# Optimization experiments

Hardware: AMD Instinct MI355X
Metric: run time of the kernel (lower is better)

The kernel has to match this reference:

```python
import jax, jax.numpy as jnp
import numpy as np

L, P = 8, 512
HID = 128
N_COARSE, N_FINE = 64, 128
LVIS_NEAR, LVIS_FAR = 1e-3, 0.5
S = 100.0  # 1 / fixed_s_recp


def _mlp_sdf(x, w0, b0, w1, b1, w2, b2, w3, b3):
    # x: [..., 3] -> sdf [...]
    h = jax.nn.relu(x @ w0 + b0)
    h = jax.nn.relu(h @ w1 + b1)
    h = jax.nn.relu(h @ w2 + b2)
    return (h @ w3 + b3)[..., 0]


def _sdf_to_w(sdf, s):
    # faithful to sdf_to_w: cdf -> alpha -> visibility weights via cumprod
    cdf = jax.nn.sigmoid(sdf * s)
    alpha = jnp.clip((cdf[..., :-1] - cdf[..., 1:]) / (cdf[..., :-1] + 1e-10), 0.0, None)
    ones = jnp.ones(alpha.shape[:-1] + (1,), alpha.dtype)
    shifted = jnp.concatenate([ones, 1.0 - alpha + 1e-10], axis=-1)
    return alpha * jnp.cumprod(shifted, axis=-1)[..., :-1]


def _sample_pdf(bins, weights, u):
    # standard NeRF importance sampling; bins [...,M+1], weights [...,M], u [...,N]
    weights = weights + 1e-5
    pdf = weights / jnp.sum(weights, axis=-1, keepdims=True)
    cdf = jnp.cumsum(pdf, axis=-1)
    cdf = jnp.concatenate([jnp.zeros_like(cdf[..., :1]), cdf], axis=-1)  # [...,M+1]
    # searchsorted (right) via broadcast compare: [...,N,M+1]
    inds = jnp.sum((u[..., None] >= cdf[..., None, :]).astype(jnp.int32), axis=-1)
    below = jnp.clip(inds - 1, 0, cdf.shape[-1] - 1)
    above = jnp.clip(inds, 0, cdf.shape[-1] - 1)
    cdf_b = jnp.take_along_axis(cdf, below, axis=-1)
    cdf_a = jnp.take_along_axis(cdf, above, axis=-1)
    bins_b = jnp.take_along_axis(bins, below, axis=-1)
    bins_a = jnp.take_along_axis(bins, above, axis=-1)
    denom = cdf_a - cdf_b
    denom = jnp.where(denom < 1e-5, jnp.ones_like(denom), denom)
    t = (u - cdf_b) / denom
    return bins_b + t * (bins_a - bins_b)


def setup_inputs() -> dict:
    key = jax.random.key(0)
    ks = jax.random.split(key, 8)

    def lin(k, fi, fo):
        return jax.random.normal(k, (fi, fo), jnp.float32) / jnp.sqrt(jnp.float32(fi))

    return {
        "pts": jax.random.normal(ks[0], (1, P, 3), jnp.float32) * 0.5,
        "light_posi": jax.random.normal(ks[1], (L, 3), jnp.float32) * 2.0,
        "u": jax.random.uniform(ks[2], (L, P, N_FINE), jnp.float32),
        "w0": lin(ks[3], 3, HID), "b0": jnp.zeros((HID,), jnp.float32),
        "w1": lin(ks[4], HID, HID), "b1": jnp.zeros((HID,), jnp.float32),
        "w2": lin(ks[5], HID, HID), "b2": jnp.zeros((HID,), jnp.float32),
        "w3": lin(ks[6], HID, 1), "b3": jnp.zeros((1,), jnp.float32),
    }


def reference(pts, light_posi, u, w0, b0, w1, b1, w2, b2, w3, b3):
    sdf = lambda x: _mlp_sdf(x, w0, b0, w1, b1, w2, b2, w3, b3)
    # pts: [1,P,3]; light_posi: [L,3]
    pts2l = light_posi[:, None, :] - pts  # [L,P,3]
    pts2l = pts2l / jnp.linalg.norm(pts2l, axis=-1, keepdims=True)
    t = jnp.linspace(0.0, 1.0 - 1.0 / N_COARSE, N_COARSE, dtype=jnp.float32)
    d_coarse = LVIS_NEAR * (1.0 - t) + LVIS_FAR * t  # [N_COARSE]
    d_coarse = jnp.broadcast_to(d_coarse, (pts2l.shape[0], pts.shape[1], N_COARSE))
    # coarse sample points: [L,P,Nc,3]
    pts_coarse = pts[:, :, None, :] + d_coarse[..., None] * pts2l[:, :, None, :]
    w_coarse = _sdf_to_w(sdf(pts_coarse), S)  # [L,P,Nc-1]
    d_fine = _sample_pdf(d_coarse, w_coarse, u)  # [L,P,Nf]
    d_all = jnp.sort(jnp.concatenate([d_coarse, d_fine], axis=-1), axis=-1)  # [L,P,Nc+Nf]
    pts_all = pts[:, :, None, :] + d_all[..., None] * pts2l[:, :, None, :]
    w_all = _sdf_to_w(sdf(pts_all), S)
    occu = jnp.sum(w_all, axis=-1)  # [L,P]
    return 1.0 - occu
```

## Files before the change

kernel.cpp:

```cpp
#include <hip/hip_runtime.h>
#include <math.h>

#define NL 8
#define NP 512
#define NC 64
#define NF 128
#define NALL 192
#define NRAY (NL * NP)
#define HID 128

typedef _Float16 half8 __attribute__((ext_vector_type(8)));
typedef _Float16 half4v __attribute__((ext_vector_type(4)));
typedef float floatx16 __attribute__((ext_vector_type(16)));

#define MFMA(a, b, c) __builtin_amdgcn_mfma_f32_32x32x16_f16((a), (b), (c), 0, 0, 0)

__device__ __forceinline__ float dcoarse_at(int i) {
    float t = (float)i * 0.015625f;
    return 1e-3f * (1.0f - t) + 0.5f * t;
}

__device__ __forceinline__ floatx16 fzero16() {
    floatx16 z;
#pragma unroll
    for (int i = 0; i < 16; ++i) z[i] = 0.f;
    return z;
}
__device__ __forceinline__ half8 hzero8() {
    half8 z;
#pragma unroll
    for (int i = 0; i < 8; ++i) z[i] = (_Float16)0.f;
    return z;
}

__global__ void prep_kernel(const float* __restrict__ w1, const float* __restrict__ w2,
                            _Float16* __restrict__ Wsp) {
    int f = blockIdx.x * 256 + threadIdx.x;
    int layer = blockIdx.y;
    const float* w = layer ? w2 : w1;
    int i = f & 7, l31 = (f >> 3) & 31, lhi = (f >> 8) & 1, ks = (f >> 9) & 7, jb = f >> 12;
    int j = jb * 32 + l31;
    int k = ks * 16 + lhi * 8 + i;
    float v = w[k * 128 + j];
    _Float16 hi = (_Float16)v;
    Wsp[(layer * 2 + 0) * 16384 + f] = hi;
    Wsp[(layer * 2 + 1) * 16384 + f] = (_Float16)(v - (float)hi);
}

template<int MODE, int FASTW>
__global__ __launch_bounds__(256, 2) void mlp_kernel(
    const float* __restrict__ pts, const float* __restrict__ lights,
    const float* __restrict__ d_all,
    const float* __restrict__ w0, const float* __restrict__ b0,
    const float* __restrict__ w1, const float* __restrict__ b1,
    const float* __restrict__ w2, const float* __restrict__ b2,
    const float* __restrict__ w3, const float* __restrict__ b3,
    const _Float16* __restrict__ Wsp,
    float* __restrict__ sdf_out)
{
    __shared__ __align__(16) _Float16 Hhi[128 * 128];
    __shared__ __align__(16) _Float16 Hlo[128 * 128];
    __shared__ _Float16 Xs[6 * 128];
    __shared__ float P2[2 * 128];

    const int tid = threadIdx.x;
    const int lane = tid & 63;
    const int wv = tid >> 6;
    const int jh = wv & 1, mh = wv >> 1;
    const int l31 = lane & 31, lhi = lane >> 5;
    const int base = blockIdx.x * 128;

    if (tid < 128) {
        int pt = base + tid;
        int ray; float d;
        if (MODE == 0) { ray = pt >> 6; d = dcoarse_at(pt & 63); }
        else           { ray = (int)((unsigned)pt / 192u); d = d_all[pt]; }
        int l = ray >> 9, p = ray & (NP - 1);
        float px = pts[p * 3 + 0], py = pts[p * 3 + 1], pz = pts[p * 3 + 2];
        float dx = lights[l * 3 + 0] - px, dy = lights[l * 3 + 1] - py, dz = lights[l * 3 + 2] - pz;
        float n = sqrtf(dx * dx + dy * dy + dz * dz);
        dx /= n; dy /= n; dz /= n;
        float xc[3] = { px + d * dx, py + d * dy, pz + d * dz };
#pragma unroll
        for (int c = 0; c < 3; ++c) {
            _Float16 h = (_Float16)xc[c];
            Xs[c * 128 + tid] = h;
            Xs[(3 + c) * 128 + tid] = (_Float16)(xc[c] - (float)h);
        }
    }
    __syncthreads();

    const int m0 = mh * 64;

    auto haddr = [&](int m, int k0) {
        return m * 128 + ((((k0 >> 3) ^ (m & 15)) << 3) | (k0 & 7));
    };

    auto store_tile = [&](const floatx16& a, int jt, int mt, const float* __restrict__ bias) {
        int m = m0 + mt * 32 + l31;
#pragma unroll
        for (int g = 0; g < 4; ++g) {
            int jg = jh * 64 + jt * 32 + 8 * g + 4 * lhi;
            half4v hq, lq;
#pragma unroll
            for (int q = 0; q < 4; ++q) {
                float v = fmaxf(a[g * 4 + q] + bias[jg + q], 0.f);
                _Float16 hi = (_Float16)v;
                hq[q] = hi;
                lq[q] = (_Float16)(v - (float)hi);
            }
            int ad = haddr(m, jg);
            *(half4v*)&Hhi[ad] = hq;
            *(half4v*)&Hlo[ad] = lq;
        }
    };

    floatx16 acc[2][2];

    {
        half8 a1h[2], a1l[2], bh1[2], bl1[2];
#pragma unroll
        for (int jt = 0; jt < 2; ++jt) { a1h[jt] = hzero8(); a1l[jt] = hzero8(); }
#pragma unroll
        for (int mt = 0; mt < 2; ++mt) { bh1[mt] = hzero8(); bl1[mt] = hzero8(); }
        if (lhi == 0) {
#pragma unroll
            for (int jt = 0; jt < 2; ++jt) {
                int j = jh * 64 + jt * 32 + l31;
#pragma unroll
                for (int c = 0; c < 3; ++c) {
                    float v = w0[c * 128 + j];
                    _Float16 hi = (_Float16)v;
                    a1h[jt][c] = hi;
                    a1l[jt][c] = (_Float16)(v - (float)hi);
                }
            }
#pragma unroll
            for (int mt = 0; mt < 2; ++mt) {
                int m = m0 + mt * 32 + l31;
#pragma unroll
                for (int c = 0; c < 3; ++c) {
                    bh1[mt][c] = Xs[c * 128 + m];
                    bl1[mt][c] = Xs[(3 + c) * 128 + m];
                }
            }
        }
#pragma unroll
        for (int jt = 0; jt < 2; ++jt)
#pragma unroll
            for (int mt = 0; mt < 2; ++mt) acc[jt][mt] = fzero16();
#pragma unroll
        for (int jt = 0; jt < 2; ++jt)
#pragma unroll
            for (int mt = 0; mt < 2; ++mt) acc[jt][mt] = MFMA(a1l[jt], bh1[mt], acc[jt][mt]);
#pragma unroll
        for (int jt = 0; jt < 2; ++jt)
#pragma unroll
            for (int mt = 0; mt < 2; ++mt) acc[jt][mt] = MFMA(a1h[jt], bl1[mt], acc[jt][mt]);
#pragma unroll
        for (int jt = 0; jt < 2; ++jt)
#pragma unroll
            for (int mt = 0; mt < 2; ++mt) acc[jt][mt] = MFMA(a1h[jt], bh1[mt], acc[jt][mt]);
#pragma unroll
        for (int jt = 0; jt < 2; ++jt)
#pragma unroll
            for (int mt = 0; mt < 2; ++mt) store_tile(acc[jt][mt], jt, mt, b0);
    }
    __syncthreads();

    auto ldA = [&](int L, int jt, int ks, half8& ah, half8& al) {
        if (FASTW) {
            int off = ((((jh * 2 + jt) * 8 + ks) * 2 + lhi) * 32 + l31) * 8;
            ah = *(const half8*)&Wsp[(L * 2 + 0) * 16384 + off];
            al = *(const half8*)&Wsp[(L * 2 + 1) * 16384 + off];
        } else {
            const float* w = L ? w2 : w1;
            int j = jh * 64 + jt * 32 + l31, k0 = ks * 16 + lhi * 8;
#pragma unroll
            for (int i = 0; i < 8; ++i) {
                float v = w[(k0 + i) * 128 + j];
                _Float16 hi = (_Float16)v;
                ah[i] = hi;
                al[i] = (_Float16)(v - (float)hi);
            }
        }
    };

    half8 bh[2][8], bl[2][8];

    auto gemm = [&](int L) {
#pragma unroll
        for (int mt = 0; mt < 2; ++mt) {
            int m = m0 + mt * 32 + l31;
#pragma unroll
            for (int ks = 0; ks < 8; ++ks) {
                int ad = haddr(m, ks * 16 + lhi * 8);
                bh[mt][ks] = *(const half8*)&Hhi[ad];
                bl[mt][ks] = *(const half8*)&Hlo[ad];
            }
        }
#pragma unroll
        for (int jt = 0; jt < 2; ++jt)
#pragma unroll
            for (int mt = 0; mt < 2; ++mt) acc[jt][mt] = fzero16();
#pragma unroll
        for (int ks = 0; ks < 8; ++ks) {
            half8 ah[2], al[2];
            ldA(L, 0, ks, ah[0], al[0]);
            ldA(L, 1, ks, ah[1], al[1]);
#pragma unroll
            for (int jt = 0; jt < 2; ++jt)
#pragma unroll
                for (int mt = 0; mt < 2; ++mt) acc[jt][mt] = MFMA(al[jt], bh[mt][ks], acc[jt][mt]);
#pragma unroll
            for (int jt = 0; jt < 2; ++jt)
#pragma unroll
                for (int mt = 0; mt < 2; ++mt) acc[jt][mt] = MFMA(ah[jt], bl[mt][ks], acc[jt][mt]);
#pragma unroll
            for (int jt = 0; jt < 2; ++jt)
#pragma unroll
                for (int mt = 0; mt < 2; ++mt) acc[jt][mt] = MFMA(ah[jt], bh[mt][ks], acc[jt][mt]);
        }
    };

    gemm(0);
    __syncthreads();
#pragma unroll
    for (int jt = 0; jt < 2; ++jt)
#pragma unroll
        for (int mt = 0; mt < 2; ++mt) store_tile(acc[jt][mt], jt, mt, b1);
    __syncthreads();

    gemm(1);
#pragma unroll
    for (int mt = 0; mt < 2; ++mt) {
        float p = 0.f;
#pragma unroll
        for (int jt = 0; jt < 2; ++jt)
#pragma unroll
            for (int g = 0; g < 4; ++g) {
                int jg = jh * 64 + jt * 32 + 8 * g + 4 * lhi;
#pragma unroll
                for (int q = 0; q < 4; ++q) {
                    float v = fmaxf(acc[jt][mt][g * 4 + q] + b2[jg + q], 0.f);
                    p = fmaf(v, w3[jg + q], p);
                }
            }
        p += __shfl_xor(p, 32);
        if (lane < 32) P2[jh * 128 + m0 + mt * 32 + l31] = p;
    }
    __syncthreads();
    if (tid < 128) sdf_out[base + tid] = b3[0] + P2[tid] + P2[128 + tid];
}

__global__ __launch_bounds__(256) void sample_kernel(
    const float* __restrict__ sdf_c, const float* __restrict__ u,
    float* __restrict__ d_all) {
    const int lane = threadIdx.x & 63, wv = threadIdx.x >> 6;
    const int ray = blockIdx.x * 4 + wv;

    float sv = sdf_c[ray * NC + lane];
    float c = 1.0f / (1.0f + expf(-100.0f * sv));
    float cn = __shfl_down(c, 1);
    bool valid = lane < 63;
    float a = valid ? fmaxf((c - cn) / (c + 1e-10f), 0.f) : 0.f;
    float sh = valid ? (1.f - a + 1e-10f) : 1.f;
    float ps = sh;
#pragma unroll
    for (int off = 1; off < 64; off <<= 1) { float o = __shfl_up(ps, off); if (lane >= off) ps *= o; }
    float T = __shfl_up(ps, 1);
    if (lane == 0) T = 1.f;
    float w = valid ? (a * T + 1e-5f) : 0.f;
    float wsum = w;
#pragma unroll
    for (int off = 1; off < 64; off <<= 1) wsum += __shfl_xor(wsum, off);
    float pdf = w / wsum;
    float cs = pdf;
#pragma unroll
    for (int off = 1; off < 64; off <<= 1) { float o = __shfl_up(cs, off); if (lane >= off) cs += o; }
    float cdfv = __shfl_up(cs, 1);
    if (lane == 0) cdfv = 0.f;

    float v[4];
    v[0] = dcoarse_at(lane);
    v[3] = __builtin_inff();
#pragma unroll
    for (int t = 0; t < 2; ++t) {
        float uu = u[ray * NF + t * 64 + lane];
        int lo = 0;
#pragma unroll
        for (int b = 32; b >= 1; b >>= 1) {
            float cm = __shfl(cdfv, lo + b);
            if (uu >= cm) lo += b;
        }
        int above = min(lo + 1, NC - 1);
        float cb = __shfl(cdfv, lo), ca = __shfl(cdfv, above);
        float bb = dcoarse_at(lo), ba = dcoarse_at(above);
        float denom = ca - cb;
        if (denom < 1e-5f) denom = 1.f;
        float tt = (uu - cb) / denom;
        v[1 + t] = bb + tt * (ba - bb);
    }

    for (int k = 2; k <= 256; k <<= 1) {
        for (int j = k >> 1; j > 0; j >>= 1) {
            if (j >= 64) {
                int tj = j >> 6;
#pragma unroll
                for (int t = 0; t < 4; ++t) {
                    if ((t & tj) == 0) {
                        int t2 = t ^ tj;
                        bool asc = (((t * 64) & k) == 0);
                        float x = v[t], y = v[t2];
                        bool sw = asc ? (x > y) : (x < y);
                        if (sw) { v[t] = y; v[t2] = x; }
                    }
                }
            } else {
#pragma unroll
                for (int t = 0; t < 4; ++t) {
                    int i = t * 64 + lane;
                    float other = __shfl_xor(v[t], j);
                    bool lower = (lane & j) == 0;
                    bool asc = ((i & k) == 0);
                    v[t] = (lower == asc) ? fminf(v[t], other) : fmaxf(v[t], other);
                }
            }
        }
    }
#pragma unroll
    for (int t = 0; t < 3; ++t) d_all[ray * NALL + t * 64 + lane] = v[t];
}

__global__ __launch_bounds__(256) void finish_kernel(
    const float* __restrict__ sdf_a, float* __restrict__ out) {
    int lane = threadIdx.x & 63, wv = threadIdx.x >> 6;
    int ray = blockIdx.x * 4 + wv;
    const float* S = sdf_a + (size_t)ray * NALL;
    float c[4];
#pragma unroll
    for (int t = 0; t < 4; ++t) {
        int i = lane * 3 + t;
        c[t] = (i < NALL) ? 1.0f / (1.0f + expf(-100.0f * S[i])) : 0.f;
    }
    float a[3], s[3];
#pragma unroll
    for (int t = 0; t < 3; ++t) {
        int i = lane * 3 + t;
        if (i < NALL - 1) {
            a[t] = fmaxf((c[t] - c[t + 1]) / (c[t] + 1e-10f), 0.f);
            s[t] = 1.f - a[t] + 1e-10f;
        } else { a[t] = 0.f; s[t] = 1.f; }
    }
    float chunk = s[0] * s[1] * s[2];
    float ps = chunk;
#pragma unroll
    for (int off = 1; off < 64; off <<= 1) {
        float o = __shfl_up(ps, off);
        if (lane >= off) ps *= o;
    }
    float T = __shfl_up(ps, 1);
    if (lane == 0) T = 1.f;
    float occ = a[0] * T;
    T *= s[0]; occ = fmaf(a[1], T, occ);
    T *= s[1]; occ = fmaf(a[2], T, occ);
#pragma unroll
    for (int off = 1; off < 64; off <<= 1) occ += __shfl_xor(occ, off);
    if (lane == 0) out[ray] = 1.f - occ;
}

extern "C" void kernel_launch(void* const* d_in, const int* in_sizes, int n_in,
                              void* d_out, int out_size, void* d_ws, size_t ws_size,
                              hipStream_t stream) {
    const float* pts = (const float*)d_in[0];
    const float* lights = (const float*)d_in[1];
    const float* u = (const float*)d_in[2];
    const float* w0 = (const float*)d_in[3];
    const float* b0 = (const float*)d_in[4];
    const float* w1 = (const float*)d_in[5];
    const float* b1 = (const float*)d_in[6];
    const float* w2 = (const float*)d_in[7];
    const float* b2 = (const float*)d_in[8];
    const float* w3 = (const float*)d_in[9];
    const float* b3 = (const float*)d_in[10];
    float* out = (float*)d_out;

    float* ws = (float*)d_ws;
    float* d_all = ws;
    float* sdf = ws + (size_t)NRAY * NALL;

    const size_t base_bytes = (size_t)2 * NRAY * NALL * 4;
    const bool fast = ws_size >= base_bytes + 4 * 16384 * sizeof(_Float16);
    _Float16* Wsp = (_Float16*)((char*)d_ws + base_bytes);

    if (fast) {
        prep_kernel<<<dim3(64, 2), 256, 0, stream>>>(w1, w2, Wsp);
        mlp_kernel<0, 1><<<(NRAY * NC) / 128, 256, 0, stream>>>(
            pts, lights, nullptr, w0, b0, w1, b1, w2, b2, w3, b3, Wsp, sdf);
        sample_kernel<<<NRAY / 4, 256, 0, stream>>>(sdf, u, d_all);
        mlp_kernel<1, 1><<<(NRAY * NALL) / 128, 256, 0, stream>>>(
            pts, lights, d_all, w0, b0, w1, b1, w2, b2, w3, b3, Wsp, sdf);
    } else {
        mlp_kernel<0, 0><<<(NRAY * NC) / 128, 256, 0, stream>>>(
            pts, lights, nullptr, w0, b0, w1, b1, w2, b2, w3, b3, nullptr, sdf);
        sample_kernel<<<NRAY / 4, 256, 0, stream>>>(sdf, u, d_all);
        mlp_kernel<1, 0><<<(NRAY * NALL) / 128, 256, 0, stream>>>(
            pts, lights, d_all, w0, b0, w1, b1, w2, b2, w3, b3, nullptr, sdf);
    }
    finish_kernel<<<NRAY / 4, 256, 0, stream>>>(sdf, out);
}
```

Before: 289.3 us.

## Reuse coarse SDF values and evaluate MLP only on fine samples via sort permutation

```diff
diff --git a/kernel.cpp b/kernel.cpp
--- a/kernel.cpp
+++ b/kernel.cpp
@@ -12,6 +12,7 @@
 typedef _Float16 half8 __attribute__((ext_vector_type(8)));
 typedef _Float16 half4v __attribute__((ext_vector_type(4)));
 typedef float floatx16 __attribute__((ext_vector_type(16)));
+typedef unsigned long long ull;
 
 #define MFMA(a, b, c) __builtin_amdgcn_mfma_f32_32x32x16_f16((a), (b), (c), 0, 0, 0)
 
@@ -50,7 +51,7 @@
 template<int MODE, int FASTW>
 __global__ __launch_bounds__(256, 2) void mlp_kernel(
     const float* __restrict__ pts, const float* __restrict__ lights,
-    const float* __restrict__ d_all,
+    const float* __restrict__ d_fine,
     const float* __restrict__ w0, const float* __restrict__ b0,
     const float* __restrict__ w1, const float* __restrict__ b1,
     const float* __restrict__ w2, const float* __restrict__ b2,
@@ -74,7 +75,7 @@
         int pt = base + tid;
         int ray; float d;
         if (MODE == 0) { ray = pt >> 6; d = dcoarse_at(pt & 63); }
-        else           { ray = (int)((unsigned)pt / 192u); d = d_all[pt]; }
+        else           { ray = pt >> 7; d = d_fine[pt]; }
         int l = ray >> 9, p = ray & (NP - 1);
         float px = pts[p * 3 + 0], py = pts[p * 3 + 1], pz = pts[p * 3 + 2];
         float dx = lights[l * 3 + 0] - px, dy = lights[l * 3 + 1] - py, dz = lights[l * 3 + 2] - pz;
@@ -255,7 +256,7 @@
 
 __global__ __launch_bounds__(256) void sample_kernel(
     const float* __restrict__ sdf_c, const float* __restrict__ u,
-    float* __restrict__ d_all) {
+    float* __restrict__ d_fine, unsigned char* __restrict__ perm8) {
     const int lane = threadIdx.x & 63, wv = threadIdx.x >> 6;
     const int ray = blockIdx.x * 4 + wv;
 
@@ -281,9 +282,7 @@
     float cdfv = __shfl_up(cs, 1);
     if (lane == 0) cdfv = 0.f;
 
-    float v[4];
-    v[0] = dcoarse_at(lane);
-    v[3] = __builtin_inff();
+    float df[2];
 #pragma unroll
     for (int t = 0; t < 2; ++t) {
         float uu = u[ray * NF + t * 64 + lane];
@@ -299,9 +298,15 @@
         float denom = ca - cb;
         if (denom < 1e-5f) denom = 1.f;
         float tt = (uu - cb) / denom;
-        v[1 + t] = bb + tt * (ba - bb);
-    }
-
+        df[t] = bb + tt * (ba - bb);
+        d_fine[ray * 128 + t * 64 + lane] = df[t];
+    }
+
+    ull v[4];
+    v[0] = ((ull)__float_as_uint(dcoarse_at(lane)) << 32) | (unsigned)lane;
+    v[1] = ((ull)__float_as_uint(df[0]) << 32) | (unsigned)(64 + lane);
+    v[2] = ((ull)__float_as_uint(df[1]) << 32) | (unsigned)(128 + lane);
+    v[3] = ((ull)0x7F800000u << 32) | 255u;
     for (int k = 2; k <= 256; k <<= 1) {
         for (int j = k >> 1; j > 0; j >>= 1) {
             if (j >= 64) {
@@ -311,7 +316,7 @@
                     if ((t & tj) == 0) {
                         int t2 = t ^ tj;
                         bool asc = (((t * 64) & k) == 0);
-                        float x = v[t], y = v[t2];
+                        ull x = v[t], y = v[t2];
                         bool sw = asc ? (x > y) : (x < y);
                         if (sw) { v[t] = y; v[t2] = x; }
                     }
@@ -320,28 +325,37 @@
 #pragma unroll
                 for (int t = 0; t < 4; ++t) {
                     int i = t * 64 + lane;
-                    float other = __shfl_xor(v[t], j);
+                    ull other = __shfl_xor(v[t], j);
                     bool lower = (lane & j) == 0;
                     bool asc = ((i & k) == 0);
-                    v[t] = (lower == asc) ? fminf(v[t], other) : fmaxf(v[t], other);
+                    bool takeMin = (lower == asc);
+                    ull mn = v[t] < other ? v[t] : other;
+                    ull mx = v[t] < other ? other : v[t];
+                    v[t] = takeMin ? mn : mx;
                 }
             }
         }
     }
 #pragma unroll
-    for (int t = 0; t < 3; ++t) d_all[ray * NALL + t * 64 + lane] = v[t];
+    for (int t = 0; t < 3; ++t)
+        perm8[ray * NALL + t * 64 + lane] = (unsigned char)(v[t] & 0xFFu);
 }
 
 __global__ __launch_bounds__(256) void finish_kernel(
-    const float* __restrict__ sdf_a, float* __restrict__ out) {
+    const float* __restrict__ sdf_c, const float* __restrict__ sdf_f,
+    const unsigned char* __restrict__ perm8, float* __restrict__ out) {
     int lane = threadIdx.x & 63, wv = threadIdx.x >> 6;
     int ray = blockIdx.x * 4 + wv;
-    const float* S = sdf_a + (size_t)ray * NALL;
+    const unsigned char* P = perm8 + (size_t)ray * NALL;
     float c[4];
 #pragma unroll
     for (int t = 0; t < 4; ++t) {
         int i = lane * 3 + t;
-        c[t] = (i < NALL) ? 1.0f / (1.0f + expf(-100.0f * S[i])) : 0.f;
+        if (i < NALL) {
+            int idx = P[i];
+            float s = (idx < 64) ? sdf_c[ray * NC + idx] : sdf_f[ray * 128 + (idx - 64)];
+            c[t] = 1.0f / (1.0f + expf(-100.0f * s));
+        } else c[t] = 0.f;
     }
     float a[3], s[3];
 #pragma unroll
@@ -385,27 +399,29 @@
     const float* b3 = (const float*)d_in[10];
     float* out = (float*)d_out;
 
-    float* ws = (float*)d_ws;
-    float* d_all = ws;
-    float* sdf = ws + (size_t)NRAY * NALL;
-
-    const size_t base_bytes = (size_t)2 * NRAY * NALL * 4;
-    const bool fast = ws_size >= base_bytes + 4 * 16384 * sizeof(_Float16);
-    _Float16* Wsp = (_Float16*)((char*)d_ws + base_bytes);
+    char* wsb = (char*)d_ws;
+    float* sdf_c = (float*)wsb;
+    float* sdf_f = (float*)(wsb + (size_t)NRAY * NC * 4);
+    float* d_fine = (float*)(wsb + (size_t)NRAY * (NC + 128) * 4);
+    unsigned char* perm8 = (unsigned char*)(wsb + (size_t)NRAY * (NC + 256) * 4);
+    _Float16* Wsp = (_Float16*)(wsb + (size_t)NRAY * (NC + 256) * 4 + (size_t)NRAY * NALL);
+    const size_t need = (size_t)NRAY * (NC + 256) * 4 + (size_t)NRAY * NALL
+                      + (size_t)4 * 16384 * sizeof(_Float16);
+    const bool fast = ws_size >= need;
 
     if (fast) {
         prep_kernel<<<dim3(64, 2), 256, 0, stream>>>(w1, w2, Wsp);
         mlp_kernel<0, 1><<<(NRAY * NC) / 128, 256, 0, stream>>>(
-            pts, lights, nullptr, w0, b0, w1, b1, w2, b2, w3, b3, Wsp, sdf);
-        sample_kernel<<<NRAY / 4, 256, 0, stream>>>(sdf, u, d_all);
-        mlp_kernel<1, 1><<<(NRAY * NALL) / 128, 256, 0, stream>>>(
-            pts, lights, d_all, w0, b0, w1, b1, w2, b2, w3, b3, Wsp, sdf);
+            pts, lights, nullptr, w0, b0, w1, b1, w2, b2, w3, b3, Wsp, sdf_c);
+        sample_kernel<<<NRAY / 4, 256, 0, stream>>>(sdf_c, u, d_fine, perm8);
+        mlp_kernel<1, 1><<<(NRAY * 128) / 128, 256, 0, stream>>>(
+            pts, lights, d_fine, w0, b0, w1, b1, w2, b2, w3, b3, Wsp, sdf_f);
     } else {
         mlp_kernel<0, 0><<<(NRAY * NC) / 128, 256, 0, stream>>>(
-            pts, lights, nullptr, w0, b0, w1, b1, w2, b2, w3, b3, nullptr, sdf);
-        sample_kernel<<<NRAY / 4, 256, 0, stream>>>(sdf, u, d_all);
-        mlp_kernel<1, 0><<<(NRAY * NALL) / 128, 256, 0, stream>>>(
-            pts, lights, d_all, w0, b0, w1, b1, w2, b2, w3, b3, nullptr, sdf);
-    }
-    finish_kernel<<<NRAY / 4, 256, 0, stream>>>(sdf, out);
-}
+            pts, lights, nullptr, w0, b0, w1, b1, w2, b2, w3, b3, nullptr, sdf_c);
+        sample_kernel<<<NRAY / 4, 256, 0, stream>>>(sdf_c, u, d_fine, perm8);
+        mlp_kernel<1, 0><<<(NRAY * 128) / 128, 256, 0, stream>>>(
+            pts, lights, d_fine, w0, b0, w1, b1, w2, b2, w3, b3, nullptr, sdf_f);
+    }
+    finish_kernel<<<NRAY / 4, 256, 0, stream>>>(sdf_c, sdf_f, perm8, out);
+}
```

Measured after the change: 253.3 us. 12.4% less time.
